# Kernel optimization log

Measured on AMD Instinct MI355X. Metric: run time of the kernel, lower is better.

## Reference

```python
import jax, jax.numpy as jnp
import numpy as np

N_NODES = 500_000
N_EDGES = 8_000_000
BN_EPS = 1e-5


def _graph_embed(src, dst, n, W_init, b_init, Wg, bg, Wt1, g1, b1, Wt2, g2, b2, Wd, bd):
    # init_graph: input is all-ones [n, 12] -> Linear(12->4); every row identical
    x_row = W_init.sum(0) + b_init                      # [4]
    h_row = jax.nn.sigmoid(x_row @ Wg + bg)             # node gating -> [7]
    h = jnp.broadcast_to(h_row, (n, h_row.shape[0]))    # [n, 7]

    # symmetric normalization, DGL TAGConv style
    deg = jnp.zeros((n,), jnp.float32).at[dst].add(1.0)
    norm = jnp.clip(deg, 1.0) ** -0.5                   # [n]

    def prop(x):  # x: [n, d] -> normalized adjacency propagation
        x = x * norm[:, None]
        agg = jnp.zeros_like(x).at[dst].add(x[src])
        return agg * norm[:, None]

    def tagconv(x, W):  # K=2: concat [h, Ah, A^2h] then linear (no bias)
        f1 = prop(x)
        f2 = prop(f1)
        return jnp.concatenate([x, f1, f2], axis=1) @ W

    def bn_relu(x, gamma, beta):  # BatchNorm1d training-mode (batch stats)
        m = x.mean(0)
        v = x.var(0)
        return jax.nn.relu((x - m) / jnp.sqrt(v + BN_EPS) * gamma + beta)

    h = bn_relu(tagconv(h, Wt1), g1, b1)
    h = bn_relu(tagconv(h, Wt2), g2, b2)
    h = h @ Wd + bd                                     # [n, 11]
    return h.mean(0)                                    # [11] graph embedding


def setup_inputs() -> dict:
    key = jax.random.key(0)
    ks = jax.random.split(key, 32)
    n, e = N_NODES, N_EDGES
    d = {
        "src1": jax.random.randint(ks[0], (e,), 0, n, dtype=jnp.int32),
        "dst1": jax.random.randint(ks[1], (e,), 0, n, dtype=jnp.int32),
        "src2": jax.random.randint(ks[2], (e,), 0, n, dtype=jnp.int32),
        "dst2": jax.random.randint(ks[3], (e,), 0, n, dtype=jnp.int32),
        "n_nodes": n,
    }
    def w(k, shape):
        return jax.random.normal(k, shape, jnp.float32) * 0.1
    # GraphEmbed params (node_emb=4, size_graph_emb=11, layers=(7,7), TAGConv K=2)
    d["W_init"] = w(ks[4], (12, 4)); d["b_init"] = w(ks[5], (4,))
    d["Wg"] = w(ks[6], (4, 7));      d["bg"] = w(ks[7], (7,))
    d["Wt1"] = w(ks[8], (21, 7))
    d["bn1_g"] = jnp.ones((7,), jnp.float32); d["bn1_b"] = jnp.zeros((7,), jnp.float32)
    d["Wt2"] = w(ks[9], (21, 7))
    d["bn2_g"] = jnp.ones((7,), jnp.float32); d["bn2_b"] = jnp.zeros((7,), jnp.float32)
    d["Wd"] = w(ks[10], (7, 11));    d["bd"] = w(ks[11], (11,))
    # GraphSimilarity params (embedding_space=11, layers=(7,7,7), 12 properties)
    d["Ws0"] = w(ks[12], (22, 7));   d["bs0"] = w(ks[13], (7,))
    d["Ws1"] = w(ks[14], (7, 7));    d["bs1"] = w(ks[15], (7,))
    d["Ws2"] = w(ks[16], (7, 7));    d["bs2"] = w(ks[17], (7,))
    d["Ws3"] = w(ks[18], (7, 7));    d["bs3"] = w(ks[19], (7,))
    d["Wsim"] = w(ks[20], (7, 12));  d["bsim"] = w(ks[21], (12,))
    return d


def reference(src1, dst1, src2, dst2, n_nodes,
              W_init, b_init, Wg, bg, Wt1, bn1_g, bn1_b, Wt2, bn2_g, bn2_b, Wd, bd,
              Ws0, bs0, Ws1, bs1, Ws2, bs2, Ws3, bs3, Wsim, bsim):
    emb = lambda s, t: _graph_embed(s, t, n_nodes, W_init, b_init, Wg, bg,
                                    Wt1, bn1_g, bn1_b, Wt2, bn2_g, bn2_b, Wd, bd)
    hg1 = emb(src1, dst1)
    hg2 = emb(src2, dst2)
    h = jnp.concatenate([hg1, hg2])[None, :]            # [1, 22]
    h = h @ Ws0 + bs0
    for W, b in ((Ws1, bs1), (Ws2, bs2), (Ws3, bs3)):
        h = jax.nn.relu(h @ W + b)
    logits = h @ Wsim + bsim                            # [1, 12]
    # sigmoid on locality logit and sigmoid on remaining diffs == elementwise sigmoid
    return jax.nn.sigmoid(logits)
```

## Files before the change

### kernel.cpp

```cpp
#include <hip/hip_runtime.h>
#include <hip/hip_bf16.h>
#include <hip/hip_fp16.h>
#include <math.h>

#define NNODES 500000
#define BN_EPS 1e-5f
#define BKT 512
#define NBKT ((NNODES + BKT - 1) / BKT)
#define EPB 16384

__device__ __forceinline__ int atomAddI(int* p, int v) {
    return __hip_atomic_fetch_add(p, v, __ATOMIC_RELAXED, __HIP_MEMORY_SCOPE_AGENT);
}
__device__ __forceinline__ void atomAddD(double* p, double v) {
    __hip_atomic_fetch_add(p, v, __ATOMIC_RELAXED, __HIP_MEMORY_SCOPE_AGENT);
}
__device__ __forceinline__ void ldsAddF(float* p, float v) {
    __hip_atomic_fetch_add(p, v, __ATOMIC_RELAXED, __HIP_MEMORY_SCOPE_WORKGROUP);
}

template<int CNT>
__device__ __forceinline__ void blk_reduce_atomic(double (&vals)[CNT], double* dst) {
    __shared__ double sh[CNT][8];
    int lane = threadIdx.x & 63, wid = threadIdx.x >> 6;
#pragma unroll
    for (int k = 0; k < CNT; ++k) {
        double v = vals[k];
#pragma unroll
        for (int o = 32; o; o >>= 1) v += __shfl_down(v, o);
        if (lane == 0) sh[k][wid] = v;
    }
    __syncthreads();
    if ((int)threadIdx.x < CNT) {
        double v = 0.0;
#pragma unroll
        for (int w = 0; w < 8; ++w) v += sh[threadIdx.x][w];
        atomAddD(dst + threadIdx.x, v);
    }
}

__global__ void k_t0(const float* __restrict__ Wi, const float* __restrict__ bi,
                     const float* __restrict__ Wg, const float* __restrict__ bg,
                     const float* __restrict__ Wt1, float* __restrict__ fs) {
    if (threadIdx.x || blockIdx.x) return;
    float xr[4];
    for (int j = 0; j < 4; ++j) {
        float s = bi[j];
        for (int k = 0; k < 12; ++k) s += Wi[k * 4 + j];
        xr[j] = s;
    }
    float hr[7];
    for (int j = 0; j < 7; ++j) {
        float s = bg[j];
        for (int k = 0; k < 4; ++k) s += xr[k] * Wg[k * 7 + j];
        hr[j] = 1.f / (1.f + expf(-s));
        fs[j] = hr[j];
    }
    for (int j = 0; j < 7; ++j) {
        float s0 = 0.f, s1 = 0.f, s2 = 0.f;
        for (int k = 0; k < 7; ++k) {
            s0 += hr[k] * Wt1[k * 7 + j];
            s1 += hr[k] * Wt1[(7 + k) * 7 + j];
            s2 += hr[k] * Wt1[(14 + k) * 7 + j];
        }
        fs[7 + j] = s0; fs[14 + j] = s1; fs[21 + j] = s2;
    }
}

__global__ void __launch_bounds__(256) k_bhist(const int* __restrict__ dst, int* __restrict__ gcnt, int E) {
    __shared__ int h[NBKT];
    for (int i = threadIdx.x; i < NBKT; i += 256) h[i] = 0;
    __syncthreads();
    int base = blockIdx.x * EPB;
#pragma unroll
    for (int k = 0; k < EPB / 1024; ++k) {
        int i4 = base + (k * 256 + threadIdx.x) * 4;
        if (i4 + 3 < E) {
            int4 d = *reinterpret_cast<const int4*>(dst + i4);
            atomicAdd(&h[d.x >> 9], 1); atomicAdd(&h[d.y >> 9], 1);
            atomicAdd(&h[d.z >> 9], 1); atomicAdd(&h[d.w >> 9], 1);
        } else {
            for (int i = i4; i < E && i < i4 + 4; ++i) atomicAdd(&h[dst[i] >> 9], 1);
        }
    }
    __syncthreads();
    for (int i = threadIdx.x; i < NBKT; i += 256)
        if (h[i]) atomAddI(gcnt + i, h[i]);
}

__global__ void __launch_bounds__(1024) k_bscan(const int* __restrict__ gcnt,
                                                int* __restrict__ bb, int* __restrict__ gcur) {
    __shared__ int sh[1024];
    int t = threadIdx.x;
    int v = (t < NBKT) ? gcnt[t] : 0;
    sh[t] = v; __syncthreads();
    for (int o = 1; o < 1024; o <<= 1) {
        int x = (t >= o) ? sh[t - o] : 0;
        __syncthreads();
        sh[t] += x;
        __syncthreads();
    }
    if (t < NBKT) { int ex = sh[t] - v; bb[t] = ex; gcur[t] = ex; }
    if (t == 0) bb[NBKT] = sh[1023];
}

__global__ void __launch_bounds__(256) k_bscat(const int* __restrict__ src, const int* __restrict__ dst,
                                               int* __restrict__ gcur, unsigned int* __restrict__ pairs, int E) {
    __shared__ int h[NBKT];
    for (int i = threadIdx.x; i < NBKT; i += 256) h[i] = 0;
    __syncthreads();
    int base = blockIdx.x * EPB;
#pragma unroll
    for (int k = 0; k < EPB / 1024; ++k) {
        int i4 = base + (k * 256 + threadIdx.x) * 4;
        if (i4 + 3 < E) {
            int4 d = *reinterpret_cast<const int4*>(dst + i4);
            atomicAdd(&h[d.x >> 9], 1); atomicAdd(&h[d.y >> 9], 1);
            atomicAdd(&h[d.z >> 9], 1); atomicAdd(&h[d.w >> 9], 1);
        } else {
            for (int i = i4; i < E && i < i4 + 4; ++i) atomicAdd(&h[dst[i] >> 9], 1);
        }
    }
    __syncthreads();
    for (int i = threadIdx.x; i < NBKT; i += 256) {
        int c = h[i];
        h[i] = c ? atomAddI(gcur + i, c) : 0;
    }
    __syncthreads();
#pragma unroll
    for (int k = 0; k < EPB / 1024; ++k) {
        int i4 = base + (k * 256 + threadIdx.x) * 4;
        if (i4 + 3 < E) {
            int4 s = *reinterpret_cast<const int4*>(src + i4);
            int4 d = *reinterpret_cast<const int4*>(dst + i4);
            int se[4] = {s.x, s.y, s.z, s.w};
            int de[4] = {d.x, d.y, d.z, d.w};
#pragma unroll
            for (int e = 0; e < 4; ++e) {
                int b = de[e] >> 9;
                int pos = atomicAdd(&h[b], 1);
                pairs[pos] = ((unsigned int)(de[e] & 511) << 19) | (unsigned int)se[e];
            }
        } else {
            for (int i = i4; i < E && i < i4 + 4; ++i) {
                int b = dst[i] >> 9;
                int pos = atomicAdd(&h[b], 1);
                pairs[pos] = ((unsigned int)(dst[i] & 511) << 19) | (unsigned int)src[i];
            }
        }
    }
}

__global__ void __launch_bounds__(512) k_deg(const unsigned int* __restrict__ pairs, const int* __restrict__ bb,
                                             float* __restrict__ nrm, float* __restrict__ sc4, int n) {
    __shared__ int deg[BKT];
    int b = blockIdx.x, t = threadIdx.x;
    deg[t] = 0;
    __syncthreads();
    int lo = bb[b], hi = bb[b + 1];
    int k = lo + t;
    for (; k + BKT < hi; k += 2 * BKT) {
        unsigned int v1 = pairs[k], v2 = pairs[k + BKT];
        atomicAdd(&deg[v1 >> 19], 1);
        atomicAdd(&deg[v2 >> 19], 1);
    }
    if (k < hi) atomicAdd(&deg[pairs[k] >> 19], 1);
    __syncthreads();
    int node = b * BKT + t;
    if (node < n) {
        float sd = sqrtf((float)(deg[t] > 0 ? deg[t] : 1));
        float nn = 1.f / sd;
        nrm[node] = nn;
        reinterpret_cast<float4*>(sc4)[node] = make_float4(0.f, 0.f, nn, sd);
    }
}

__global__ void __launch_bounds__(512) k_s1(const unsigned int* __restrict__ pairs, const int* __restrict__ bb,
                                            const float* __restrict__ nrm, float* __restrict__ s1,
                                            float* __restrict__ s1n, float* __restrict__ sc4, int n) {
    __shared__ float acc[BKT];
    int b = blockIdx.x, t = threadIdx.x;
    acc[t] = 0.f;
    __syncthreads();
    int lo = bb[b], hi = bb[b + 1];
    int k = lo + t;
    for (; k + BKT < hi; k += 2 * BKT) {
        unsigned int v1 = pairs[k], v2 = pairs[k + BKT];
        float g1 = nrm[v1 & 0x7FFFF], g2 = nrm[v2 & 0x7FFFF];
        ldsAddF(&acc[v1 >> 19], g1);
        ldsAddF(&acc[v2 >> 19], g2);
    }
    if (k < hi) { unsigned int v = pairs[k]; ldsAddF(&acc[v >> 19], nrm[v & 0x7FFFF]); }
    __syncthreads();
    int node = b * BKT + t;
    if (node < n) {
        float nn = nrm[node], v1 = acc[t] * nn;
        s1[node] = v1; s1n[node] = v1 * nn;
        sc4[(size_t)node * 4 + 0] = v1;
    }
}

__global__ void __launch_bounds__(512) k_s2(const unsigned int* __restrict__ pairs, const int* __restrict__ bb,
                                            const float* __restrict__ nrm, const float* __restrict__ s1,
                                            const float* __restrict__ s1n, float* __restrict__ sc4,
                                            double* __restrict__ ds, int n) {
    __shared__ float acc[BKT];
    int b = blockIdx.x, t = threadIdx.x;
    acc[t] = 0.f;
    __syncthreads();
    int lo = bb[b], hi = bb[b + 1];
    int k = lo + t;
    for (; k + BKT < hi; k += 2 * BKT) {
        unsigned int v1 = pairs[k], v2 = pairs[k + BKT];
        float g1 = s1n[v1 & 0x7FFFF], g2 = s1n[v2 & 0x7FFFF];
        ldsAddF(&acc[v1 >> 19], g1);
        ldsAddF(&acc[v2 >> 19], g2);
    }
    if (k < hi) { unsigned int v = pairs[k]; ldsAddF(&acc[v >> 19], s1n[v & 0x7FFFF]); }
    __syncthreads();
    double m[5] = {0, 0, 0, 0, 0};
    int node = b * BKT + t;
    if (node < n) {
        float nn = nrm[node], v2 = acc[t] * nn;
        sc4[(size_t)node * 4 + 1] = v2;
        float v1 = s1[node];
        m[0] += v1; m[1] += v2;
        m[2] += (double)v1 * (double)v1;
        m[3] += (double)v2 * (double)v2;
        m[4] += (double)v1 * (double)v2;
    }
    blk_reduce_atomic<5>(m, ds);
}

__global__ void k_t1(const double* __restrict__ ds, const float* __restrict__ fs,
                     const float* __restrict__ g1, const float* __restrict__ b1, float* __restrict__ fsg) {
    if (threadIdx.x || blockIdx.x) return;
    const double inv_n = 1.0 / (double)NNODES;
    float mu1 = (float)(ds[0] * inv_n), mu2 = (float)(ds[1] * inv_n);
    float V11 = (float)(ds[2] * inv_n) - mu1 * mu1;
    float V22 = (float)(ds[3] * inv_n) - mu2 * mu2;
    float V12 = (float)(ds[4] * inv_n) - mu1 * mu2;
    for (int j = 0; j < 7; ++j) {
        float a1 = fs[14 + j], a2 = fs[21 + j];
        float var = a1 * a1 * V11 + a2 * a2 * V22 + 2.f * a1 * a2 * V12;
        float ig = (1.f / sqrtf(var + BN_EPS)) * g1[j];
        fsg[j]      = b1[j] - (mu1 * a1 + mu2 * a2) * ig;
        fsg[7 + j]  = a1 * ig;
        fsg[14 + j] = a2 * ig;
    }
}

__global__ void __launch_bounds__(512) k_f1(const unsigned int* __restrict__ pairs, const int* __restrict__ bb,
                                            const float* __restrict__ nrm, const float* __restrict__ sc4,
                                            const float* __restrict__ fsg, float* __restrict__ f1nh, int n) {
    __shared__ float a[7][BKT];
    int b = blockIdx.x, t = threadIdx.x;
    float dc[21];
#pragma unroll
    for (int j = 0; j < 21; ++j) dc[j] = fsg[j];
#pragma unroll
    for (int j = 0; j < 7; ++j) a[j][t] = 0.f;
    __syncthreads();
    int lo = bb[b], hi = bb[b + 1];
    int k = lo + t;
    for (; k + BKT < hi; k += 2 * BKT) {
        unsigned int v1 = pairs[k], v2 = pairs[k + BKT];
        float4 r1 = reinterpret_cast<const float4*>(sc4)[v1 & 0x7FFFF];
        float4 r2 = reinterpret_cast<const float4*>(sc4)[v2 & 0x7FFFF];
        int d1 = v1 >> 19, d2 = v2 >> 19;
#pragma unroll
        for (int j = 0; j < 7; ++j) {
            float h = fmaxf(dc[j] + r1.x * dc[7 + j] + r1.y * dc[14 + j], 0.f) * r1.z;
            ldsAddF(&a[j][d1], h);
        }
#pragma unroll
        for (int j = 0; j < 7; ++j) {
            float h = fmaxf(dc[j] + r2.x * dc[7 + j] + r2.y * dc[14 + j], 0.f) * r2.z;
            ldsAddF(&a[j][d2], h);
        }
    }
    if (k < hi) {
        unsigned int v = pairs[k];
        float4 r = reinterpret_cast<const float4*>(sc4)[v & 0x7FFFF];
        int dl = v >> 19;
#pragma unroll
        for (int j = 0; j < 7; ++j) {
            float h = fmaxf(dc[j] + r.x * dc[7 + j] + r.y * dc[14 + j], 0.f) * r.z;
            ldsAddF(&a[j][dl], h);
        }
    }
    __syncthreads();
    int node = b * BKT + t;
    if (node < n) {
        float nn = nrm[node], sc = nn * nn;
        __half2 hh[4];
        hh[0] = __floats2half2_rn(a[0][t] * sc, a[1][t] * sc);
        hh[1] = __floats2half2_rn(a[2][t] * sc, a[3][t] * sc);
        hh[2] = __floats2half2_rn(a[4][t] * sc, a[5][t] * sc);
        hh[3] = __floats2half2_rn(a[6][t] * sc, 0.f);
        reinterpret_cast<float4*>(f1nh)[node] = *reinterpret_cast<float4*>(hh);
    }
}

__global__ void __launch_bounds__(512) k_x2f(const unsigned int* __restrict__ pairs, const int* __restrict__ bb,
                                             const float* __restrict__ sc4, const float* __restrict__ fsg,
                                             const float* __restrict__ f1nh, const float* __restrict__ Wt2,
                                             float* __restrict__ x2o, double* __restrict__ ds, int n) {
    __shared__ float a[7][BKT];
    __shared__ float w[147];
    int b = blockIdx.x, t = threadIdx.x;
    for (int k = t; k < 147; k += 512) w[k] = Wt2[k];
    float dc[21];
#pragma unroll
    for (int j = 0; j < 21; ++j) dc[j] = fsg[j];
#pragma unroll
    for (int j = 0; j < 7; ++j) a[j][t] = 0.f;
    __syncthreads();
    int lo = bb[b], hi = bb[b + 1];
    int k = lo + t;
    for (; k + BKT < hi; k += 2 * BKT) {
        unsigned int v1 = pairs[k], v2 = pairs[k + BKT];
        float4 raw1 = reinterpret_cast<const float4*>(f1nh)[v1 & 0x7FFFF];
        float4 raw2 = reinterpret_cast<const float4*>(f1nh)[v2 & 0x7FFFF];
        int d1 = v1 >> 19, d2 = v2 >> 19;
        {
            const __half2* hp = reinterpret_cast<const __half2*>(&raw1);
            float2 q0 = __half22float2(hp[0]), q1 = __half22float2(hp[1]);
            float2 q2 = __half22float2(hp[2]), q3 = __half22float2(hp[3]);
            ldsAddF(&a[0][d1], q0.x); ldsAddF(&a[1][d1], q0.y); ldsAddF(&a[2][d1], q1.x);
            ldsAddF(&a[3][d1], q1.y); ldsAddF(&a[4][d1], q2.x); ldsAddF(&a[5][d1], q2.y);
            ldsAddF(&a[6][d1], q3.x);
        }
        {
            const __half2* hp = reinterpret_cast<const __half2*>(&raw2);
            float2 q0 = __half22float2(hp[0]), q1 = __half22float2(hp[1]);
            float2 q2 = __half22float2(hp[2]), q3 = __half22float2(hp[3]);
            ldsAddF(&a[0][d2], q0.x); ldsAddF(&a[1][d2], q0.y); ldsAddF(&a[2][d2], q1.x);
            ldsAddF(&a[3][d2], q1.y); ldsAddF(&a[4][d2], q2.x); ldsAddF(&a[5][d2], q2.y);
            ldsAddF(&a[6][d2], q3.x);
        }
    }
    if (k < hi) {
        unsigned int v = pairs[k];
        float4 raw = reinterpret_cast<const float4*>(f1nh)[v & 0x7FFFF];
        int dl = v >> 19;
        const __half2* hp = reinterpret_cast<const __half2*>(&raw);
        float2 q0 = __half22float2(hp[0]), q1 = __half22float2(hp[1]);
        float2 q2 = __half22float2(hp[2]), q3 = __half22float2(hp[3]);
        ldsAddF(&a[0][dl], q0.x); ldsAddF(&a[1][dl], q0.y); ldsAddF(&a[2][dl], q1.x);
        ldsAddF(&a[3][dl], q1.y); ldsAddF(&a[4][dl], q2.x); ldsAddF(&a[5][dl], q2.y);
        ldsAddF(&a[6][dl], q3.x);
    }
    __syncthreads();
    double sx[7] = {0, 0, 0, 0, 0, 0, 0}, sq[7] = {0, 0, 0, 0, 0, 0, 0};
    int node = b * BKT + t;
    if (node < n) {
        float4 s = reinterpret_cast<const float4*>(sc4)[node];
        float S1 = s.x, S2 = s.y, Nn = s.z, rn = s.w;
        float h1[7];
#pragma unroll
        for (int kk = 0; kk < 7; ++kk) h1[kk] = fmaxf(dc[kk] + S1 * dc[7 + kk] + S2 * dc[14 + kk], 0.f);
        float4 raw = reinterpret_cast<const float4*>(f1nh)[node];
        const __half2* hp = reinterpret_cast<const __half2*>(&raw);
        float2 q0 = __half22float2(hp[0]), q1 = __half22float2(hp[1]);
        float2 q2 = __half22float2(hp[2]), q3 = __half22float2(hp[3]);
        float f1p[7] = {q0.x * rn, q0.y * rn, q1.x * rn, q1.y * rn, q2.x * rn, q2.y * rn, q3.x * rn};
        float f2p[7];
#pragma unroll
        for (int kk = 0; kk < 7; ++kk) f2p[kk] = a[kk][t] * Nn;
        float x2[8];
#pragma unroll
        for (int j = 0; j < 7; ++j) {
            float sacc = 0.f;
#pragma unroll
            for (int kk = 0; kk < 7; ++kk)
                sacc += h1[kk] * w[kk * 7 + j] + f1p[kk] * w[(7 + kk) * 7 + j] + f2p[kk] * w[(14 + kk) * 7 + j];
            x2[j] = sacc;
            sx[j] += sacc; sq[j] += (double)sacc * (double)sacc;
        }
        x2[7] = 0.f;
        float4* q = reinterpret_cast<float4*>(x2o + (size_t)node * 8);
        q[0] = make_float4(x2[0], x2[1], x2[2], x2[3]);
        q[1] = make_float4(x2[4], x2[5], x2[6], x2[7]);
    }
    double acc[14];
#pragma unroll
    for (int j = 0; j < 7; ++j) { acc[j] = sx[j]; acc[7 + j] = sq[j]; }
    blk_reduce_atomic<14>(acc, ds + 5);
}

__global__ void k_t2(const double* __restrict__ ds, const float* __restrict__ g2,
                     const float* __restrict__ b2, float* __restrict__ fsg) {
    if (threadIdx.x || blockIdx.x) return;
    const double inv_n = 1.0 / (double)NNODES;
    for (int j = 0; j < 7; ++j) {
        float m = (float)(ds[5 + j] * inv_n);
        float v = (float)(ds[12 + j] * inv_n) - m * m;
        float ig = (1.f / sqrtf(v + BN_EPS)) * g2[j];
        fsg[21 + j] = b2[j] - m * ig;
        fsg[28 + j] = ig;
    }
}

__global__ void __launch_bounds__(512) k_h2sum(const float* __restrict__ x2o, const float* __restrict__ fsg,
                                               double* __restrict__ ds, int n) {
    float c0[7], c1[7];
#pragma unroll
    for (int j = 0; j < 7; ++j) { c0[j] = fsg[21 + j]; c1[j] = fsg[28 + j]; }
    double acc[7] = {0, 0, 0, 0, 0, 0, 0};
    for (int i = blockIdx.x * blockDim.x + threadIdx.x; i < n; i += gridDim.x * blockDim.x) {
        const float4* p = reinterpret_cast<const float4*>(x2o + (size_t)i * 8);
        float4 a = p[0], b = p[1];
        float x[7] = {a.x, a.y, a.z, a.w, b.x, b.y, b.z};
#pragma unroll
        for (int j = 0; j < 7; ++j) acc[j] += (double)fmaxf(x[j] * c1[j] + c0[j], 0.f);
    }
    blk_reduce_atomic<7>(acc, ds + 19);
}

__global__ void k_final(const double* __restrict__ ds, const float* __restrict__ Wd, const float* __restrict__ bd,
                        const float* __restrict__ Ws0, const float* __restrict__ bs0,
                        const float* __restrict__ Ws1, const float* __restrict__ bs1,
                        const float* __restrict__ Ws2, const float* __restrict__ bs2,
                        const float* __restrict__ Ws3, const float* __restrict__ bs3,
                        const float* __restrict__ Wsim, const float* __restrict__ bsim,
                        float* __restrict__ out) {
    if (threadIdx.x || blockIdx.x) return;
    const double inv_n = 1.0 / (double)NNODES;
    float v[22];
    for (int g = 0; g < 2; ++g) {
        float hm[7];
        for (int j = 0; j < 7; ++j) hm[j] = (float)(ds[g * 26 + 19 + j] * inv_n);
        for (int r = 0; r < 11; ++r) {
            float s = bd[r];
            for (int j = 0; j < 7; ++j) s += hm[j] * Wd[j * 11 + r];
            v[g * 11 + r] = s;
        }
    }
    float h[7], h2[7];
    for (int j = 0; j < 7; ++j) {
        float s = bs0[j];
        for (int k = 0; k < 22; ++k) s += v[k] * Ws0[k * 7 + j];
        h[j] = s;
    }
    const float* Ws[3] = {Ws1, Ws2, Ws3};
    const float* bs[3] = {bs1, bs2, bs3};
    for (int l = 0; l < 3; ++l) {
        for (int j = 0; j < 7; ++j) {
            float s = bs[l][j];
            for (int k = 0; k < 7; ++k) s += h[k] * Ws[l][k * 7 + j];
            h2[j] = fmaxf(s, 0.f);
        }
        for (int j = 0; j < 7; ++j) h[j] = h2[j];
    }
    for (int r = 0; r < 12; ++r) {
        float s = bsim[r];
        for (int j = 0; j < 7; ++j) s += h[j] * Wsim[j * 12 + r];
        out[r] = 1.f / (1.f + expf(-s));
    }
}

extern "C" void kernel_launch(void* const* d_in, const int* in_sizes, int n_in,
                              void* d_out, int out_size, void* d_ws, size_t ws_size,
                              hipStream_t stream) {
    const int E = in_sizes[0];
    const int n = NNODES;
    const int* src1 = (const int*)d_in[0];
    const int* dst1 = (const int*)d_in[1];
    const int* src2 = (const int*)d_in[2];
    const int* dst2 = (const int*)d_in[3];
    const float* W_init = (const float*)d_in[5];
    const float* b_init = (const float*)d_in[6];
    const float* Wg  = (const float*)d_in[7];
    const float* bg  = (const float*)d_in[8];
    const float* Wt1 = (const float*)d_in[9];
    const float* g1  = (const float*)d_in[10];
    const float* b1  = (const float*)d_in[11];
    const float* Wt2 = (const float*)d_in[12];
    const float* g2  = (const float*)d_in[13];
    const float* b2  = (const float*)d_in[14];
    const float* Wd  = (const float*)d_in[15];
    const float* bd  = (const float*)d_in[16];
    const float* Ws0 = (const float*)d_in[17];
    const float* bs0 = (const float*)d_in[18];
    const float* Ws1 = (const float*)d_in[19];
    const float* bs1 = (const float*)d_in[20];
    const float* Ws2 = (const float*)d_in[21];
    const float* bs2 = (const float*)d_in[22];
    const float* Ws3 = (const float*)d_in[23];
    const float* bs3 = (const float*)d_in[24];
    const float* Wsim = (const float*)d_in[25];
    const float* bsim = (const float*)d_in[26];

    double* dscal = (double*)d_ws;
    float* fscal  = (float*)(dscal + 52);
    float* F      = (float*)((char*)d_ws + 1024);
    float* nrm  = F;
    float* s1   = F + (size_t)n;
    float* s1n  = F + 2 * (size_t)n;
    float* sc4  = F + 3 * (size_t)n;
    float* f1nh = F + 7 * (size_t)n;
    float* x2o  = F + 11 * (size_t)n;
    int*   gcnt = (int*)(F + 19 * (size_t)n);
    int*   bb   = gcnt + NBKT;
    int*   gcur = bb + NBKT + 1;
    unsigned int* pairs = (unsigned int*)(gcur + NBKT);

    const int EB = (E + EPB - 1) / EPB;

    hipMemsetAsync(dscal, 0, 52 * sizeof(double), stream);
    k_t0<<<1, 1, 0, stream>>>(W_init, b_init, Wg, bg, Wt1, fscal);

    for (int g = 0; g < 2; ++g) {
        const int* src = g ? src2 : src1;
        const int* dst = g ? dst2 : dst1;
        float* fsg  = fscal + 28 + g * 35;
        double* dsg = dscal + g * 26;

        hipMemsetAsync(gcnt, 0, NBKT * sizeof(int), stream);
        k_bhist<<<EB, 256, 0, stream>>>(dst, gcnt, E);
        k_bscan<<<1, 1024, 0, stream>>>(gcnt, bb, gcur);
        k_bscat<<<EB, 256, 0, stream>>>(src, dst, gcur, pairs, E);

        k_deg<<<NBKT, 512, 0, stream>>>(pairs, bb, nrm, sc4, n);
        k_s1 <<<NBKT, 512, 0, stream>>>(pairs, bb, nrm, s1, s1n, sc4, n);
        k_s2 <<<NBKT, 512, 0, stream>>>(pairs, bb, nrm, s1, s1n, sc4, dsg, n);
        k_t1<<<1, 1, 0, stream>>>(dsg, fscal, g1, b1, fsg);
        k_f1 <<<NBKT, 512, 0, stream>>>(pairs, bb, nrm, sc4, fsg, f1nh, n);
        k_x2f<<<NBKT, 512, 0, stream>>>(pairs, bb, sc4, fsg, f1nh, Wt2, x2o, dsg, n);
        k_t2<<<1, 1, 0, stream>>>(dsg, g2, b2, fsg);
        k_h2sum<<<512, 512, 0, stream>>>(x2o, fsg, dsg, n);
    }
    k_final<<<1, 1, 0, stream>>>(dscal, Wd, bd, Ws0, bs0, Ws1, bs1, Ws2, bs2, Ws3, bs3,
                                 Wsim, bsim, (float*)d_out);
}
```

Before: 2.057 ms.

## Pack gather operands into half-precision table, unroll edge loops 4x, widen bucketing blocks

Adds an 8-byte half-precision per-node table (S1, S2, norm) written in k_s2, so k_f1 gathers 8 bytes per edge instead of a 16-byte float4. All bucket-processing edge loops are unrolled from 2 to 4 independent loads to expose more memory-level parallelism. Histogram and scatter kernels move from 256 to 512 threads per block. The half-precision S1/S2/norm values lose precision in the first-layer propagation and add a small extra write in k_s2.

```diff
diff --git a/kernel.cpp b/kernel.cpp
--- a/kernel.cpp
+++ b/kernel.cpp
@@ -67,14 +67,14 @@
     }
 }
 
-__global__ void __launch_bounds__(256) k_bhist(const int* __restrict__ dst, int* __restrict__ gcnt, int E) {
+__global__ void __launch_bounds__(512) k_bhist(const int* __restrict__ dst, int* __restrict__ gcnt, int E) {
     __shared__ int h[NBKT];
-    for (int i = threadIdx.x; i < NBKT; i += 256) h[i] = 0;
+    for (int i = threadIdx.x; i < NBKT; i += 512) h[i] = 0;
     __syncthreads();
     int base = blockIdx.x * EPB;
 #pragma unroll
-    for (int k = 0; k < EPB / 1024; ++k) {
-        int i4 = base + (k * 256 + threadIdx.x) * 4;
+    for (int k = 0; k < EPB / 2048; ++k) {
+        int i4 = base + (k * 512 + threadIdx.x) * 4;
         if (i4 + 3 < E) {
             int4 d = *reinterpret_cast<const int4*>(dst + i4);
             atomicAdd(&h[d.x >> 9], 1); atomicAdd(&h[d.y >> 9], 1);
@@ -84,7 +84,7 @@
         }
     }
     __syncthreads();
-    for (int i = threadIdx.x; i < NBKT; i += 256)
+    for (int i = threadIdx.x; i < NBKT; i += 512)
         if (h[i]) atomAddI(gcnt + i, h[i]);
 }
 
@@ -104,15 +104,15 @@
     if (t == 0) bb[NBKT] = sh[1023];
 }
 
-__global__ void __launch_bounds__(256) k_bscat(const int* __restrict__ src, const int* __restrict__ dst,
+__global__ void __launch_bounds__(512) k_bscat(const int* __restrict__ src, const int* __restrict__ dst,
                                                int* __restrict__ gcur, unsigned int* __restrict__ pairs, int E) {
     __shared__ int h[NBKT];
-    for (int i = threadIdx.x; i < NBKT; i += 256) h[i] = 0;
+    for (int i = threadIdx.x; i < NBKT; i += 512) h[i] = 0;
     __syncthreads();
     int base = blockIdx.x * EPB;
 #pragma unroll
-    for (int k = 0; k < EPB / 1024; ++k) {
-        int i4 = base + (k * 256 + threadIdx.x) * 4;
+    for (int k = 0; k < EPB / 2048; ++k) {
+        int i4 = base + (k * 512 + threadIdx.x) * 4;
         if (i4 + 3 < E) {
             int4 d = *reinterpret_cast<const int4*>(dst + i4);
             atomicAdd(&h[d.x >> 9], 1); atomicAdd(&h[d.y >> 9], 1);
@@ -122,14 +122,14 @@
         }
     }
     __syncthreads();
-    for (int i = threadIdx.x; i < NBKT; i += 256) {
+    for (int i = threadIdx.x; i < NBKT; i += 512) {
         int c = h[i];
         h[i] = c ? atomAddI(gcur + i, c) : 0;
     }
     __syncthreads();
 #pragma unroll
-    for (int k = 0; k < EPB / 1024; ++k) {
-        int i4 = base + (k * 256 + threadIdx.x) * 4;
+    for (int k = 0; k < EPB / 2048; ++k) {
+        int i4 = base + (k * 512 + threadIdx.x) * 4;
         if (i4 + 3 < E) {
             int4 s = *reinterpret_cast<const int4*>(src + i4);
             int4 d = *reinterpret_cast<const int4*>(dst + i4);
@@ -159,12 +159,13 @@
     __syncthreads();
     int lo = bb[b], hi = bb[b + 1];
     int k = lo + t;
-    for (; k + BKT < hi; k += 2 * BKT) {
+    for (; k + 3 * BKT < hi; k += 4 * BKT) {
         unsigned int v1 = pairs[k], v2 = pairs[k + BKT];
-        atomicAdd(&deg[v1 >> 19], 1);
-        atomicAdd(&deg[v2 >> 19], 1);
-    }
-    if (k < hi) atomicAdd(&deg[pairs[k] >> 19], 1);
+        unsigned int v3 = pairs[k + 2 * BKT], v4 = pairs[k + 3 * BKT];
+        atomicAdd(&deg[v1 >> 19], 1); atomicAdd(&deg[v2 >> 19], 1);
+        atomicAdd(&deg[v3 >> 19], 1); atomicAdd(&deg[v4 >> 19], 1);
+    }
+    for (; k < hi; k += BKT) atomicAdd(&deg[pairs[k] >> 19], 1);
     __syncthreads();
     int node = b * BKT + t;
     if (node < n) {
@@ -184,13 +185,15 @@
     __syncthreads();
     int lo = bb[b], hi = bb[b + 1];
     int k = lo + t;
-    for (; k + BKT < hi; k += 2 * BKT) {
+    for (; k + 3 * BKT < hi; k += 4 * BKT) {
         unsigned int v1 = pairs[k], v2 = pairs[k + BKT];
+        unsigned int v3 = pairs[k + 2 * BKT], v4 = pairs[k + 3 * BKT];
         float g1 = nrm[v1 & 0x7FFFF], g2 = nrm[v2 & 0x7FFFF];
-        ldsAddF(&acc[v1 >> 19], g1);
-        ldsAddF(&acc[v2 >> 19], g2);
-    }
-    if (k < hi) { unsigned int v = pairs[k]; ldsAddF(&acc[v >> 19], nrm[v & 0x7FFFF]); }
+        float g3 = nrm[v3 & 0x7FFFF], g4 = nrm[v4 & 0x7FFFF];
+        ldsAddF(&acc[v1 >> 19], g1); ldsAddF(&acc[v2 >> 19], g2);
+        ldsAddF(&acc[v3 >> 19], g3); ldsAddF(&acc[v4 >> 19], g4);
+    }
+    for (; k < hi; k += BKT) { unsigned int v = pairs[k]; ldsAddF(&acc[v >> 19], nrm[v & 0x7FFFF]); }
     __syncthreads();
     int node = b * BKT + t;
     if (node < n) {
@@ -203,20 +206,22 @@
 __global__ void __launch_bounds__(512) k_s2(const unsigned int* __restrict__ pairs, const int* __restrict__ bb,
                                             const float* __restrict__ nrm, const float* __restrict__ s1,
                                             const float* __restrict__ s1n, float* __restrict__ sc4,
-                                            double* __restrict__ ds, int n) {
+                                            float* __restrict__ sch, double* __restrict__ ds, int n) {
     __shared__ float acc[BKT];
     int b = blockIdx.x, t = threadIdx.x;
     acc[t] = 0.f;
     __syncthreads();
     int lo = bb[b], hi = bb[b + 1];
     int k = lo + t;
-    for (; k + BKT < hi; k += 2 * BKT) {
+    for (; k + 3 * BKT < hi; k += 4 * BKT) {
         unsigned int v1 = pairs[k], v2 = pairs[k + BKT];
+        unsigned int v3 = pairs[k + 2 * BKT], v4 = pairs[k + 3 * BKT];
         float g1 = s1n[v1 & 0x7FFFF], g2 = s1n[v2 & 0x7FFFF];
-        ldsAddF(&acc[v1 >> 19], g1);
-        ldsAddF(&acc[v2 >> 19], g2);
-    }
-    if (k < hi) { unsigned int v = pairs[k]; ldsAddF(&acc[v >> 19], s1n[v & 0x7FFFF]); }
+        float g3 = s1n[v3 & 0x7FFFF], g4 = s1n[v4 & 0x7FFFF];
+        ldsAddF(&acc[v1 >> 19], g1); ldsAddF(&acc[v2 >> 19], g2);
+        ldsAddF(&acc[v3 >> 19], g3); ldsAddF(&acc[v4 >> 19], g4);
+    }
+    for (; k < hi; k += BKT) { unsigned int v = pairs[k]; ldsAddF(&acc[v >> 19], s1n[v & 0x7FFFF]); }
     __syncthreads();
     double m[5] = {0, 0, 0, 0, 0};
     int node = b * BKT + t;
@@ -224,6 +229,11 @@
         float nn = nrm[node], v2 = acc[t] * nn;
         sc4[(size_t)node * 4 + 1] = v2;
         float v1 = s1[node];
+        __half2 p0 = __floats2half2_rn(v1, v2);
+        __half2 p1 = __floats2half2_rn(nn, 0.f);
+        float2 packed = make_float2(__uint_as_float(*(unsigned int*)&p0),
+                                    __uint_as_float(*(unsigned int*)&p1));
+        reinterpret_cast<float2*>(sch)[node] = packed;
         m[0] += v1; m[1] += v2;
         m[2] += (double)v1 * (double)v1;
         m[3] += (double)v2 * (double)v2;
@@ -250,8 +260,20 @@
     }
 }
 
+__device__ __forceinline__ void f1_edge(const float2 r, const float* dc, float (&sarr)[7][BKT], int dl) {
+    unsigned int u0 = __float_as_uint(r.x), u1 = __float_as_uint(r.y);
+    __half2 h0 = *(__half2*)&u0, h1v = *(__half2*)&u1;
+    float2 q0 = __half22float2(h0), q1 = __half22float2(h1v);
+    float S1 = q0.x, S2 = q0.y, Nn = q1.x;
+#pragma unroll
+    for (int j = 0; j < 7; ++j) {
+        float h = fmaxf(dc[j] + S1 * dc[7 + j] + S2 * dc[14 + j], 0.f) * Nn;
+        ldsAddF(&sarr[j][dl], h);
+    }
+}
+
 __global__ void __launch_bounds__(512) k_f1(const unsigned int* __restrict__ pairs, const int* __restrict__ bb,
-                                            const float* __restrict__ nrm, const float* __restrict__ sc4,
+                                            const float* __restrict__ nrm, const float* __restrict__ sch,
                                             const float* __restrict__ fsg, float* __restrict__ f1nh, int n) {
     __shared__ float a[7][BKT];
     int b = blockIdx.x, t = threadIdx.x;
@@ -263,31 +285,22 @@
     __syncthreads();
     int lo = bb[b], hi = bb[b + 1];
     int k = lo + t;
-    for (; k + BKT < hi; k += 2 * BKT) {
+    for (; k + 3 * BKT < hi; k += 4 * BKT) {
         unsigned int v1 = pairs[k], v2 = pairs[k + BKT];
-        float4 r1 = reinterpret_cast<const float4*>(sc4)[v1 & 0x7FFFF];
-        float4 r2 = reinterpret_cast<const float4*>(sc4)[v2 & 0x7FFFF];
-        int d1 = v1 >> 19, d2 = v2 >> 19;
-#pragma unroll
-        for (int j = 0; j < 7; ++j) {
-            float h = fmaxf(dc[j] + r1.x * dc[7 + j] + r1.y * dc[14 + j], 0.f) * r1.z;
-            ldsAddF(&a[j][d1], h);
-        }
-#pragma unroll
-        for (int j = 0; j < 7; ++j) {
-            float h = fmaxf(dc[j] + r2.x * dc[7 + j] + r2.y * dc[14 + j], 0.f) * r2.z;
-            ldsAddF(&a[j][d2], h);
-        }
-    }
-    if (k < hi) {
+        unsigned int v3 = pairs[k + 2 * BKT], v4 = pairs[k + 3 * BKT];
+        float2 r1 = reinterpret_cast<const float2*>(sch)[v1 & 0x7FFFF];
+        float2 r2 = reinterpret_cast<const float2*>(sch)[v2 & 0x7FFFF];
+        float2 r3 = reinterpret_cast<const float2*>(sch)[v3 & 0x7FFFF];
+        float2 r4 = reinterpret_cast<const float2*>(sch)[v4 & 0x7FFFF];
+        f1_edge(r1, dc, a, v1 >> 19);
+        f1_edge(r2, dc, a, v2 >> 19);
+        f1_edge(r3, dc, a, v3 >> 19);
+        f1_edge(r4, dc, a, v4 >> 19);
+    }
+    for (; k < hi; k += BKT) {
         unsigned int v = pairs[k];
-        float4 r = reinterpret_cast<const float4*>(sc4)[v & 0x7FFFF];
-        int dl = v >> 19;
-#pragma unroll
-        for (int j = 0; j < 7; ++j) {
-            float h = fmaxf(dc[j] + r.x * dc[7 + j] + r.y * dc[14 + j], 0.f) * r.z;
-            ldsAddF(&a[j][dl], h);
-        }
+        float2 r = reinterpret_cast<const float2*>(sch)[v & 0x7FFFF];
+        f1_edge(r, dc, a, v >> 19);
     }
     __syncthreads();
     int node = b * BKT + t;
@@ -302,6 +315,15 @@
     }
 }
 
+__device__ __forceinline__ void x2_edge(const float4 raw, float (&sarr)[7][BKT], int dl) {
+    const __half2* hp = reinterpret_cast<const __half2*>(&raw);
+    float2 q0 = __half22float2(hp[0]), q1 = __half22float2(hp[1]);
+    float2 q2 = __half22float2(hp[2]), q3 = __half22float2(hp[3]);
+    ldsAddF(&sarr[0][dl], q0.x); ldsAddF(&sarr[1][dl], q0.y); ldsAddF(&sarr[2][dl], q1.x);
+    ldsAddF(&sarr[3][dl], q1.y); ldsAddF(&sarr[4][dl], q2.x); ldsAddF(&sarr[5][dl], q2.y);
+    ldsAddF(&sarr[6][dl], q3.x);
+}
+
 __global__ void __launch_bounds__(512) k_x2f(const unsigned int* __restrict__ pairs, const int* __restrict__ bb,
                                              const float* __restrict__ sc4, const float* __restrict__ fsg,
                                              const float* __restrict__ f1nh, const float* __restrict__ Wt2,
@@ -318,38 +340,22 @@
     __syncthreads();
     int lo = bb[b], hi = bb[b + 1];
     int k = lo + t;
-    for (; k + BKT < hi; k += 2 * BKT) {
+    for (; k + 3 * BKT < hi; k += 4 * BKT) {
         unsigned int v1 = pairs[k], v2 = pairs[k + BKT];
-        float4 raw1 = reinterpret_cast<const float4*>(f1nh)[v1 & 0x7FFFF];
-        float4 raw2 = reinterpret_cast<const float4*>(f1nh)[v2 & 0x7FFFF];
-        int d1 = v1 >> 19, d2 = v2 >> 19;
-        {
-            const __half2* hp = reinterpret_cast<const __half2*>(&raw1);
-            float2 q0 = __half22float2(hp[0]), q1 = __half22float2(hp[1]);
-            float2 q2 = __half22float2(hp[2]), q3 = __half22float2(hp[3]);
-            ldsAddF(&a[0][d1], q0.x); ldsAddF(&a[1][d1], q0.y); ldsAddF(&a[2][d1], q1.x);
-            ldsAddF(&a[3][d1], q1.y); ldsAddF(&a[4][d1], q2.x); ldsAddF(&a[5][d1], q2.y);
-            ldsAddF(&a[6][d1], q3.x);
-        }
-        {
-            const __half2* hp = reinterpret_cast<const __half2*>(&raw2);
-            float2 q0 = __half22float2(hp[0]), q1 = __half22float2(hp[1]);
-            float2 q2 = __half22float2(hp[2]), q3 = __half22float2(hp[3]);
-            ldsAddF(&a[0][d2], q0.x); ldsAddF(&a[1][d2], q0.y); ldsAddF(&a[2][d2], q1.x);
-            ldsAddF(&a[3][d2], q1.y); ldsAddF(&a[4][d2], q2.x); ldsAddF(&a[5][d2], q2.y);
-            ldsAddF(&a[6][d2], q3.x);
-        }
-    }
-    if (k < hi) {
+        unsigned int v3 = pairs[k + 2 * BKT], v4 = pairs[k + 3 * BKT];
+        float4 r1 = reinterpret_cast<const float4*>(f1nh)[v1 & 0x7FFFF];
+        float4 r2 = reinterpret_cast<const float4*>(f1nh)[v2 & 0x7FFFF];
+        float4 r3 = reinterpret_cast<const float4*>(f1nh)[v3 & 0x7FFFF];
+        float4 r4 = reinterpret_cast<const float4*>(f1nh)[v4 & 0x7FFFF];
+        x2_edge(r1, a, v1 >> 19);
+        x2_edge(r2, a, v2 >> 19);
+        x2_edge(r3, a, v3 >> 19);
+        x2_edge(r4, a, v4 >> 19);
+    }
+    for (; k < hi; k += BKT) {
         unsigned int v = pairs[k];
         float4 raw = reinterpret_cast<const float4*>(f1nh)[v & 0x7FFFF];
-        int dl = v >> 19;
-        const __half2* hp = reinterpret_cast<const __half2*>(&raw);
-        float2 q0 = __half22float2(hp[0]), q1 = __half22float2(hp[1]);
-        float2 q2 = __half22float2(hp[2]), q3 = __half22float2(hp[3]);
-        ldsAddF(&a[0][dl], q0.x); ldsAddF(&a[1][dl], q0.y); ldsAddF(&a[2][dl], q1.x);
-        ldsAddF(&a[3][dl], q1.y); ldsAddF(&a[4][dl], q2.x); ldsAddF(&a[5][dl], q2.y);
-        ldsAddF(&a[6][dl], q3.x);
+        x2_edge(raw, a, v >> 19);
     }
     __syncthreads();
     double sx[7] = {0, 0, 0, 0, 0, 0, 0}, sq[7] = {0, 0, 0, 0, 0, 0, 0};
@@ -499,9 +505,10 @@
     float* s1   = F + (size_t)n;
     float* s1n  = F + 2 * (size_t)n;
     float* sc4  = F + 3 * (size_t)n;
-    float* f1nh = F + 7 * (size_t)n;
-    float* x2o  = F + 11 * (size_t)n;
-    int*   gcnt = (int*)(F + 19 * (size_t)n);
+    float* sch  = F + 7 * (size_t)n;
+    float* f1nh = F + 9 * (size_t)n;
+    float* x2o  = F + 13 * (size_t)n;
+    int*   gcnt = (int*)(F + 21 * (size_t)n);
     int*   bb   = gcnt + NBKT;
     int*   gcur = bb + NBKT + 1;
     unsigned int* pairs = (unsigned int*)(gcur + NBKT);
@@ -518,15 +525,15 @@
         double* dsg = dscal + g * 26;
 
         hipMemsetAsync(gcnt, 0, NBKT * sizeof(int), stream);
-        k_bhist<<<EB, 256, 0, stream>>>(dst, gcnt, E);
+        k_bhist<<<EB, 512, 0, stream>>>(dst, gcnt, E);
         k_bscan<<<1, 1024, 0, stream>>>(gcnt, bb, gcur);
-        k_bscat<<<EB, 256, 0, stream>>>(src, dst, gcur, pairs, E);
+        k_bscat<<<EB, 512, 0, stream>>>(src, dst, gcur, pairs, E);
 
         k_deg<<<NBKT, 512, 0, stream>>>(pairs, bb, nrm, sc4, n);
         k_s1 <<<NBKT, 512, 0, stream>>>(pairs, bb, nrm, s1, s1n, sc4, n);
-        k_s2 <<<NBKT, 512, 0, stream>>>(pairs, bb, nrm, s1, s1n, sc4, dsg, n);
+        k_s2 <<<NBKT, 512, 0, stream>>>(pairs, bb, nrm, s1, s1n, sc4, sch, dsg, n);
         k_t1<<<1, 1, 0, stream>>>(dsg, fscal, g1, b1, fsg);
-        k_f1 <<<NBKT, 512, 0, stream>>>(pairs, bb, nrm, sc4, fsg, f1nh, n);
+        k_f1 <<<NBKT, 512, 0, stream>>>(pairs, bb, nrm, sch, fsg, f1nh, n);
         k_x2f<<<NBKT, 512, 0, stream>>>(pairs, bb, sc4, fsg, f1nh, Wt2, x2o, dsg, n);
         k_t2<<<1, 1, 0, stream>>>(dsg, g2, b2, fsg);
         k_h2sum<<<512, 512, 0, stream>>>(x2o, fsg, dsg, n);
```

Measured after the change: 2.011 ms. 2.2% less time.
